# Kernel tuning notes

Measured on AMD Instinct MI355X. Metric: run time of the kernel, lower is better.

Reference implementation:

```python
import jax, jax.numpy as jnp
import numpy as np

RHO = 1.0
EPSILON = 0.1
N_ITERS = 5
EPS = 1e-08


def setup_inputs() -> dict:
    key = jax.random.key(0)
    k1, k2, k3 = jax.random.split(key, 3)
    B, H, M, N, D = 16, 16, 256, 576, 1024
    # student cross-attention weights: positive, rows roughly sum to 1 (post-softmax in the real model)
    sa = jax.random.uniform(k1, (B, H, M, N), dtype=jnp.float32) + 1e-3
    student_attn = sa / sa.sum(axis=-1, keepdims=True)
    visual_feats = jax.random.normal(k2, (B, N, D), dtype=jnp.float32)
    text_feats = jax.random.normal(k3, (B, M, D), dtype=jnp.float32)
    text_mask = jnp.ones((B, M), dtype=jnp.float32)
    return {"student_attn": student_attn, "visual_feats": visual_feats,
            "text_feats": text_feats, "text_mask": text_mask}


def _l2norm(x):
    return x / jnp.sqrt(jnp.sum(x * x, axis=-1, keepdims=True) + 1e-12)


def _teacher_plan(x, y, y_mask):
    # x: (B,N,D) visual, y: (B,M,D) text, y_mask: (B,M)
    B, N, D = x.shape
    M = y.shape[1]
    x_n = _l2norm(x)
    y_n = _l2norm(y)
    cost = 1.0 - jnp.einsum('bmd,bnd->bmn', y_n, x_n)          # (B,M,N)
    mu = jnp.full((B, N, 1), 1.0 / N, dtype=x.dtype)            # visual marginal (column vec)
    nu = (y_mask / (jnp.sum(y_mask, axis=1, keepdims=True) + EPS))[:, :, None]  # (B,M,1)
    K = jnp.exp(-cost / EPSILON)                                # (B,M,N)
    fi = RHO / (RHO + EPSILON)
    u = jnp.ones((B, M, 1), dtype=x.dtype)
    v = jnp.ones((B, N, 1), dtype=x.dtype)
    for _ in range(N_ITERS):
        Kv = jnp.einsum('bmn,bnk->bmk', K, v)                   # (B,M,1)
        u = (nu / (Kv + EPS)) ** fi
        Ktu = jnp.einsum('bmn,bmk->bnk', K, u)                  # (B,N,1)
        v = (mu / (Ktu + EPS)) ** fi
    P = u * K * jnp.swapaxes(v, 1, 2)                           # (B,M,N)
    return P / (jnp.sum(P, axis=-1, keepdims=True) + EPS)


def reference(student_attn, visual_feats, text_feats, text_mask):
    teacher = jax.lax.stop_gradient(_teacher_plan(visual_feats, text_feats, text_mask))
    teacher = teacher[:, None, :, :]                            # (B,1,M,N)
    loss = -jnp.sum(teacher * jnp.log(student_attn + EPS), axis=-1)  # (B,H,M)
    loss = loss * text_mask[:, None, :]
    return jnp.mean(loss)
```

## Files before the change

### kernel.cpp

```cpp
#include <hip/hip_runtime.h>
#include <math.h>

#define B_ 16
#define H_ 16
#define M_ 256
#define N_ 576
#define D_ 1024
#define BK 64
#define LDS_STRIDE (BK + 8)
#define NROWS (B_ * N_ + B_ * M_)

constexpr float EPS_ = 1e-8f;
constexpr float FI_ = 0.90909090909090906f;

typedef __bf16 bf16x8 __attribute__((ext_vector_type(8)));
typedef float f32x4 __attribute__((ext_vector_type(4)));

__device__ __forceinline__ float wave_reduce(float v) {
#pragma unroll
  for (int o = 32; o > 0; o >>= 1) v += __shfl_down(v, o, 64);
  return v;
}

__device__ __forceinline__ unsigned short f2bf(float f) {
  union { float f; unsigned u; } a; a.f = f;
  unsigned r = a.u + 0x7fff + ((a.u >> 16) & 1);
  return (unsigned short)(r >> 16);
}

__device__ __forceinline__ float bf2f(unsigned short u) {
  union { unsigned u; float f; } a; a.u = ((unsigned)u) << 16;
  return a.f;
}

__global__ __launch_bounds__(256) void sumlog_kernel(const float* __restrict__ student,
                                                     float* __restrict__ SL) {
  const int m = blockIdx.x;
  const int b = blockIdx.y;
  const int t = threadIdx.x;
  if (t >= N_ / 4) return;
  const float* st = student + ((size_t)b * H_ * M_ + m) * N_ + t * 4;
  float4 acc = {0.f, 0.f, 0.f, 0.f};
#pragma unroll
  for (int h = 0; h < H_; ++h) {
    float4 s4 = *(const float4*)&st[(size_t)h * M_ * N_];
    acc.x += __logf(s4.x + EPS_);
    acc.y += __logf(s4.y + EPS_);
    acc.z += __logf(s4.z + EPS_);
    acc.w += __logf(s4.w + EPS_);
  }
  *(float4*)&SL[((size_t)b * M_ + m) * N_ + t * 4] = acc;
}

__global__ __launch_bounds__(256) void prep_kernel(const float* __restrict__ vis,
                                                   const float* __restrict__ txt,
                                                   const float* __restrict__ mask,
                                                   unsigned short* __restrict__ xb,
                                                   unsigned short* __restrict__ yb,
                                                   float* __restrict__ masksum) {
  const int bid = blockIdx.x;
  const int lane = threadIdx.x & 63;
  if (bid < NROWS / 4) {
    int wave = bid * 4 + (threadIdx.x >> 6);
    const float* src;
    unsigned short* dst;
    if (wave < B_ * N_) {
      src = vis + (size_t)wave * D_;
      dst = xb + (size_t)wave * D_;
    } else {
      int r = wave - B_ * N_;
      src = txt + (size_t)r * D_;
      dst = yb + (size_t)r * D_;
    }
    float4 v[4];
    float s = 0.f;
#pragma unroll
    for (int it = 0; it < 4; ++it) {
      v[it] = *(const float4*)&src[it * 256 + lane * 4];
      s += v[it].x * v[it].x + v[it].y * v[it].y + v[it].z * v[it].z + v[it].w * v[it].w;
    }
    s = wave_reduce(s);
    s = __shfl(s, 0, 64);
    float inv = rsqrtf(s + 1e-12f);
#pragma unroll
    for (int it = 0; it < 4; ++it) {
      ushort4 pk;
      pk.x = f2bf(v[it].x * inv);
      pk.y = f2bf(v[it].y * inv);
      pk.z = f2bf(v[it].z * inv);
      pk.w = f2bf(v[it].w * inv);
      *(ushort4*)&dst[it * 256 + lane * 4] = pk;
    }
  } else {
    int b = (bid - NROWS / 4) * 4 + (threadIdx.x >> 6);
    float4 mv = *(const float4*)&mask[b * M_ + lane * 4];
    float s = wave_reduce(mv.x + mv.y + mv.z + mv.w);
    if (lane == 0) masksum[b] = s;
  }
}

__global__ __launch_bounds__(256) void gemm_k_mfma(const unsigned short* __restrict__ xb,
                                                   const unsigned short* __restrict__ yb,
                                                   unsigned short* __restrict__ Kw) {
  __shared__ unsigned short As[64][LDS_STRIDE];
  __shared__ unsigned short Bs[64][LDS_STRIDE];
  const int b = blockIdx.z;
  const int m0 = blockIdx.y * 64;
  const int n0 = blockIdx.x * 64;
  const unsigned short* Y = yb + (size_t)b * M_ * D_;
  const unsigned short* X = xb + (size_t)b * N_ * D_;
  const int t = threadIdx.x;
  const int lane = t & 63;
  const int w = t >> 6;
  const int wm = (w & 1) * 32;
  const int wn = (w >> 1) * 32;
  const int lr = t >> 3;
  const int lc = (t & 7) * 8;
  const int fr = lane & 15;
  const int fk = (lane >> 4) * 8;

  f32x4 acc[2][2] = {};
  for (int k0 = 0; k0 < D_; k0 += BK) {
#pragma unroll
    for (int p = 0; p < 2; ++p) {
      *(uint4*)&As[lr + 32 * p][lc] = *(const uint4*)&Y[(size_t)(m0 + lr + 32 * p) * D_ + k0 + lc];
      *(uint4*)&Bs[lr + 32 * p][lc] = *(const uint4*)&X[(size_t)(n0 + lr + 32 * p) * D_ + k0 + lc];
    }
    __syncthreads();
#pragma unroll
    for (int ks = 0; ks < BK; ks += 32) {
      bf16x8 a[2], bfr[2];
#pragma unroll
      for (int i = 0; i < 2; ++i) {
        a[i] = *(const bf16x8*)&As[wm + i * 16 + fr][ks + fk];
        bfr[i] = *(const bf16x8*)&Bs[wn + i * 16 + fr][ks + fk];
      }
#pragma unroll
      for (int i = 0; i < 2; ++i)
#pragma unroll
        for (int j = 0; j < 2; ++j)
          acc[i][j] = __builtin_amdgcn_mfma_f32_16x16x32_bf16(a[i], bfr[j], acc[i][j], 0, 0, 0);
    }
    __syncthreads();
  }

  const int cm = (lane >> 4) * 4;
  const int cn = lane & 15;
#pragma unroll
  for (int i = 0; i < 2; ++i)
#pragma unroll
    for (int j = 0; j < 2; ++j)
#pragma unroll
      for (int rg = 0; rg < 4; ++rg) {
        int m = m0 + wm + i * 16 + cm + rg;
        int n = n0 + wn + j * 16 + cn;
        Kw[((size_t)b * M_ + m) * N_ + n] = f2bf(expf(10.f * (acc[i][j][rg] - 1.f)));
      }
}


__global__ __launch_bounds__(256) void sink_u_first(const unsigned short* __restrict__ Kw,
                                                    const float* __restrict__ mask,
                                                    const float* __restrict__ masksum,
                                                    float* __restrict__ u) {
  const int b = blockIdx.y;
  const int row = blockIdx.x * 4 + (threadIdx.x >> 6);
  const int lane = threadIdx.x & 63;
  const unsigned short* rowp = Kw + ((size_t)b * M_ + row) * N_;
  float s = 0.f;
#pragma unroll
  for (int k = 0; k < 9; ++k) s += bf2f(rowp[lane + 64 * k]);
  s = wave_reduce(s);
  if (lane == 0) {
    int idx = b * M_ + row;
    float nu = mask[idx] / (masksum[b] + EPS_);
    u[idx] = powf(nu / (s + EPS_), FI_);
  }
}

__global__ __launch_bounds__(256) void sink_u(const unsigned short* __restrict__ Kw,
                                              const float* __restrict__ v,
                                              const float* __restrict__ mask,
                                              const float* __restrict__ masksum,
                                              float* __restrict__ u) {
  const int b = blockIdx.y;
  const int row = blockIdx.x * 4 + (threadIdx.x >> 6);
  const int lane = threadIdx.x & 63;
  const unsigned short* rowp = Kw + ((size_t)b * M_ + row) * N_;
  const float* vb = v + b * N_;
  float s = 0.f;
#pragma unroll
  for (int k = 0; k < 9; ++k) s += bf2f(rowp[lane + 64 * k]) * vb[lane + 64 * k];
  s = wave_reduce(s);
  if (lane == 0) {
    int idx = b * M_ + row;
    float nu = mask[idx] / (masksum[b] + EPS_);
    u[idx] = powf(nu / (s + EPS_), FI_);
  }
}

__global__ __launch_bounds__(256) void sink_v(const unsigned short* __restrict__ Kw,
                                              const float* __restrict__ u,
                                              float* __restrict__ v) {
  __shared__ float part[4][64];
  const int b = blockIdx.y;
  const int n0 = blockIdx.x * 64;
  const int col = n0 + (threadIdx.x & 63);
  const int g = threadIdx.x >> 6;
  const unsigned short* Kb = Kw + (size_t)b * M_ * N_;
  const float* ub = u + b * M_;
  float s = 0.f;
#pragma unroll 8
  for (int m = g * 64; m < (g + 1) * 64; ++m) s += bf2f(Kb[(size_t)m * N_ + col]) * ub[m];
  part[g][threadIdx.x & 63] = s;
  __syncthreads();
  if (threadIdx.x < 64) {
    float tot = part[0][threadIdx.x] + part[1][threadIdx.x] +
                part[2][threadIdx.x] + part[3][threadIdx.x];
    v[b * N_ + n0 + threadIdx.x] = powf((1.f / (float)N_) / (tot + EPS_), FI_);
  }
}

__global__ __launch_bounds__(256) void finloss_kernel(const unsigned short* __restrict__ Kw,
                                                      const float* __restrict__ SL,
                                                      const float* __restrict__ v,
                                                      const float* __restrict__ mask,
                                                      float* __restrict__ partial) {
  __shared__ float red[2][4];
  const int m = blockIdx.x;
  const int b = blockIdx.y;
  const int t = threadIdx.x;
  float s1 = 0.f, s2 = 0.f;
  if (t < N_ / 4) {
    const unsigned short* kp = Kw + ((size_t)b * M_ + m) * N_ + t * 4;
    ushort4 k4 = *(const ushort4*)kp;
    float4 v4 = *(const float4*)&v[b * N_ + t * 4];
    float4 sl4 = *(const float4*)&SL[((size_t)b * M_ + m) * N_ + t * 4];
    float kv0 = bf2f(k4.x) * v4.x, kv1 = bf2f(k4.y) * v4.y;
    float kv2 = bf2f(k4.z) * v4.z, kv3 = bf2f(k4.w) * v4.w;
    s1 = kv0 + kv1 + kv2 + kv3;
    s2 = kv0 * sl4.x + kv1 * sl4.y + kv2 * sl4.z + kv3 * sl4.w;
  }
  s1 = wave_reduce(s1);
  s2 = wave_reduce(s2);
  if ((t & 63) == 0) { red[0][t >> 6] = s1; red[1][t >> 6] = s2; }
  __syncthreads();
  if (t == 0) {
    float S1 = red[0][0] + red[0][1] + red[0][2] + red[0][3];
    float S2 = red[1][0] + red[1][1] + red[1][2] + red[1][3];
    int row = b * M_ + m;
    partial[row] = -mask[row] * S2 / ((S1 + EPS_) * (float)(B_ * H_ * M_));
  }
}

__global__ __launch_bounds__(256) void reduce_kernel(const float* __restrict__ partial,
                                                     float* __restrict__ out) {
  __shared__ float red[4];
  float s = 0.f;
  for (int i = threadIdx.x; i < B_ * M_; i += 256) s += partial[i];
  s = wave_reduce(s);
  if ((threadIdx.x & 63) == 0) red[threadIdx.x >> 6] = s;
  __syncthreads();
  if (threadIdx.x == 0) out[0] = red[0] + red[1] + red[2] + red[3];
}

extern "C" void kernel_launch(void* const* d_in, const int* in_sizes, int n_in,
                              void* d_out, int out_size, void* d_ws, size_t ws_size,
                              hipStream_t stream) {
  const float* student = (const float*)d_in[0];
  const float* vis = (const float*)d_in[1];
  const float* txt = (const float*)d_in[2];
  const float* mask = (const float*)d_in[3];
  float* out = (float*)d_out;

  char* p = (char*)d_ws;
  unsigned short* Kb = (unsigned short*)p; p += (size_t)B_ * M_ * N_ * 2;
  unsigned short* xb = (unsigned short*)p; p += (size_t)B_ * N_ * D_ * 2;
  unsigned short* yb = (unsigned short*)p; p += (size_t)B_ * M_ * D_ * 2;
  float* SL = (float*)p;      p += (size_t)B_ * M_ * N_ * 4;
  float* vv = (float*)p;      p += B_ * N_ * 4;
  float* uu = (float*)p;      p += B_ * M_ * 4;
  float* msum = (float*)p;    p += B_ * 4;
  float* partial = (float*)p; p += B_ * M_ * 4;

  sumlog_kernel<<<dim3(M_, B_), 256, 0, stream>>>(student, SL);

  prep_kernel<<<NROWS / 4 + 4, 256, 0, stream>>>(vis, txt, mask, xb, yb, msum);
  gemm_k_mfma<<<dim3(N_ / 64, M_ / 64, B_), 256, 0, stream>>>(xb, yb, Kb);

  sink_u_first<<<dim3(M_ / 4, B_), 256, 0, stream>>>(Kb, mask, msum, uu);
  sink_v<<<dim3(N_ / 64, B_), 256, 0, stream>>>(Kb, uu, vv);
  for (int it = 1; it < 5; ++it) {
    sink_u<<<dim3(M_ / 4, B_), 256, 0, stream>>>(Kb, vv, mask, msum, uu);
    sink_v<<<dim3(N_ / 64, B_), 256, 0, stream>>>(Kb, uu, vv);
  }

  finloss_kernel<<<dim3(M_, B_), 256, 0, stream>>>(Kb, SL, vv, mask, partial);
  reduce_kernel<<<1, 256, 0, stream>>>(partial, out);
}
```

Before: 335.7 us.

## Fuse Sinkhorn iterations into one per-batch kernel co-scheduled with sumlog

Replaces the ten separate Sinkhorn u/v kernel launches with a single kernel in which one 1024-thread block per batch runs all five iterations, keeping u and v in shared memory. The student log-sum work moves into extra blocks of the same launch, so it runs alongside the serial Sinkhorn blocks instead of as its own kernel. This removes launch overhead and global round-trips for u and v. In exchange only 16 blocks do the Sinkhorn work, which leaves little parallelism per batch, and the sumlog part now runs after the GEMM rather than before it.

```diff
diff --git a/kernel.cpp b/kernel.cpp
--- a/kernel.cpp
+++ b/kernel.cpp
@@ -10,6 +10,9 @@
 #define LDS_STRIDE (BK + 8)
 #define NROWS (B_ * N_ + B_ * M_)
 
+#define SINK_BLOCKS B_
+#define SUMLOG_BLOCKS ((B_ * M_ * N_ / 4) / 1024)
+
 constexpr float EPS_ = 1e-8f;
 constexpr float FI_ = 0.90909090909090906f;
 
@@ -31,25 +34,6 @@
 __device__ __forceinline__ float bf2f(unsigned short u) {
   union { unsigned u; float f; } a; a.u = ((unsigned)u) << 16;
   return a.f;
-}
-
-__global__ __launch_bounds__(256) void sumlog_kernel(const float* __restrict__ student,
-                                                     float* __restrict__ SL) {
-  const int m = blockIdx.x;
-  const int b = blockIdx.y;
-  const int t = threadIdx.x;
-  if (t >= N_ / 4) return;
-  const float* st = student + ((size_t)b * H_ * M_ + m) * N_ + t * 4;
-  float4 acc = {0.f, 0.f, 0.f, 0.f};
-#pragma unroll
-  for (int h = 0; h < H_; ++h) {
-    float4 s4 = *(const float4*)&st[(size_t)h * M_ * N_];
-    acc.x += __logf(s4.x + EPS_);
-    acc.y += __logf(s4.y + EPS_);
-    acc.z += __logf(s4.z + EPS_);
-    acc.w += __logf(s4.w + EPS_);
-  }
-  *(float4*)&SL[((size_t)b * M_ + m) * N_ + t * 4] = acc;
 }
 
 __global__ __launch_bounds__(256) void prep_kernel(const float* __restrict__ vis,
@@ -158,67 +142,83 @@
       }
 }
 
-
-__global__ __launch_bounds__(256) void sink_u_first(const unsigned short* __restrict__ Kw,
-                                                    const float* __restrict__ mask,
-                                                    const float* __restrict__ masksum,
-                                                    float* __restrict__ u) {
-  const int b = blockIdx.y;
-  const int row = blockIdx.x * 4 + (threadIdx.x >> 6);
-  const int lane = threadIdx.x & 63;
-  const unsigned short* rowp = Kw + ((size_t)b * M_ + row) * N_;
-  float s = 0.f;
-#pragma unroll
-  for (int k = 0; k < 9; ++k) s += bf2f(rowp[lane + 64 * k]);
-  s = wave_reduce(s);
-  if (lane == 0) {
-    int idx = b * M_ + row;
-    float nu = mask[idx] / (masksum[b] + EPS_);
-    u[idx] = powf(nu / (s + EPS_), FI_);
-  }
-}
-
-__global__ __launch_bounds__(256) void sink_u(const unsigned short* __restrict__ Kw,
-                                              const float* __restrict__ v,
-                                              const float* __restrict__ mask,
-                                              const float* __restrict__ masksum,
-                                              float* __restrict__ u) {
-  const int b = blockIdx.y;
-  const int row = blockIdx.x * 4 + (threadIdx.x >> 6);
-  const int lane = threadIdx.x & 63;
-  const unsigned short* rowp = Kw + ((size_t)b * M_ + row) * N_;
-  const float* vb = v + b * N_;
-  float s = 0.f;
-#pragma unroll
-  for (int k = 0; k < 9; ++k) s += bf2f(rowp[lane + 64 * k]) * vb[lane + 64 * k];
-  s = wave_reduce(s);
-  if (lane == 0) {
-    int idx = b * M_ + row;
-    float nu = mask[idx] / (masksum[b] + EPS_);
-    u[idx] = powf(nu / (s + EPS_), FI_);
-  }
-}
-
-__global__ __launch_bounds__(256) void sink_v(const unsigned short* __restrict__ Kw,
-                                              const float* __restrict__ u,
-                                              float* __restrict__ v) {
-  __shared__ float part[4][64];
-  const int b = blockIdx.y;
-  const int n0 = blockIdx.x * 64;
-  const int col = n0 + (threadIdx.x & 63);
-  const int g = threadIdx.x >> 6;
+__global__ __launch_bounds__(1024) void sink_sumlog_kernel(
+    const unsigned short* __restrict__ Kw,
+    const float* __restrict__ mask,
+    const float* __restrict__ masksum,
+    const float* __restrict__ student,
+    float* __restrict__ SL,
+    float* __restrict__ vv) {
+  if (blockIdx.x >= SINK_BLOCKS) {
+    const int t = threadIdx.x;
+    const int idx = (blockIdx.x - SINK_BLOCKS) * 1024 + t;
+    const int b = idx / (M_ * N_ / 4);
+    const int cb = idx - b * (M_ * N_ / 4);
+    const float* st = student + (size_t)b * H_ * M_ * N_ + (size_t)cb * 4;
+    float4 acc = {0.f, 0.f, 0.f, 0.f};
+#pragma unroll
+    for (int h = 0; h < H_; ++h) {
+      float4 s4 = *(const float4*)&st[(size_t)h * M_ * N_];
+      acc.x += __logf(s4.x + EPS_);
+      acc.y += __logf(s4.y + EPS_);
+      acc.z += __logf(s4.z + EPS_);
+      acc.w += __logf(s4.w + EPS_);
+    }
+    *(float4*)&SL[(size_t)b * M_ * N_ + (size_t)cb * 4] = acc;
+    return;
+  }
+
+  __shared__ float u_s[M_];
+  __shared__ float v_s[N_];
+  __shared__ float nu_s[M_];
+  __shared__ float vp[4][N_];
+  const int b = blockIdx.x;
+  const int t = threadIdx.x;
+  const int lane = t & 63;
+  const int w = t >> 6;
   const unsigned short* Kb = Kw + (size_t)b * M_ * N_;
-  const float* ub = u + b * M_;
-  float s = 0.f;
+
+  if (t < M_) nu_s[t] = mask[b * M_ + t] / (masksum[b] + EPS_);
+  if (t < N_) v_s[t] = 1.f;
+  __syncthreads();
+
+  for (int it = 0; it < 5; ++it) {
+#pragma unroll 2
+    for (int r = 0; r < 16; ++r) {
+      const int m = w * 16 + r;
+      const unsigned short* rp = Kb + (size_t)m * N_;
+      float s = 0.f;
+#pragma unroll
+      for (int k = 0; k < 9; ++k) s += bf2f(rp[lane + 64 * k]) * v_s[lane + 64 * k];
+      s = wave_reduce(s);
+      if (lane == 0) u_s[m] = powf(nu_s[m] / (s + EPS_), FI_);
+    }
+    __syncthreads();
+
+    if (t < 576) {
+      const int q = t / 144;
+      const int c4 = (t - q * 144) * 4;
+      float s0 = 0.f, s1 = 0.f, s2 = 0.f, s3 = 0.f;
 #pragma unroll 8
-  for (int m = g * 64; m < (g + 1) * 64; ++m) s += bf2f(Kb[(size_t)m * N_ + col]) * ub[m];
-  part[g][threadIdx.x & 63] = s;
-  __syncthreads();
-  if (threadIdx.x < 64) {
-    float tot = part[0][threadIdx.x] + part[1][threadIdx.x] +
-                part[2][threadIdx.x] + part[3][threadIdx.x];
-    v[b * N_ + n0 + threadIdx.x] = powf((1.f / (float)N_) / (tot + EPS_), FI_);
-  }
+      for (int m = q * 64; m < q * 64 + 64; ++m) {
+        ushort4 k4 = *(const ushort4*)&Kb[(size_t)m * N_ + c4];
+        const float um = u_s[m];
+        s0 += bf2f(k4.x) * um;
+        s1 += bf2f(k4.y) * um;
+        s2 += bf2f(k4.z) * um;
+        s3 += bf2f(k4.w) * um;
+      }
+      float4 r4 = {s0, s1, s2, s3};
+      *(float4*)&vp[q][c4] = r4;
+    }
+    __syncthreads();
+    if (t < N_) {
+      float tot = vp[0][t] + vp[1][t] + vp[2][t] + vp[3][t];
+      v_s[t] = powf((1.f / (float)N_) / (tot + EPS_), FI_);
+    }
+    __syncthreads();
+  }
+  if (t < N_) vv[b * N_ + t] = v_s[t];
 }
 
 __global__ __launch_bounds__(256) void finloss_kernel(const unsigned short* __restrict__ Kw,
@@ -279,21 +279,14 @@
   unsigned short* yb = (unsigned short*)p; p += (size_t)B_ * M_ * D_ * 2;
   float* SL = (float*)p;      p += (size_t)B_ * M_ * N_ * 4;
   float* vv = (float*)p;      p += B_ * N_ * 4;
-  float* uu = (float*)p;      p += B_ * M_ * 4;
   float* msum = (float*)p;    p += B_ * 4;
   float* partial = (float*)p; p += B_ * M_ * 4;
 
-  sumlog_kernel<<<dim3(M_, B_), 256, 0, stream>>>(student, SL);
-
   prep_kernel<<<NROWS / 4 + 4, 256, 0, stream>>>(vis, txt, mask, xb, yb, msum);
   gemm_k_mfma<<<dim3(N_ / 64, M_ / 64, B_), 256, 0, stream>>>(xb, yb, Kb);
 
-  sink_u_first<<<dim3(M_ / 4, B_), 256, 0, stream>>>(Kb, mask, msum, uu);
-  sink_v<<<dim3(N_ / 64, B_), 256, 0, stream>>>(Kb, uu, vv);
-  for (int it = 1; it < 5; ++it) {
-    sink_u<<<dim3(M_ / 4, B_), 256, 0, stream>>>(Kb, vv, mask, msum, uu);
-    sink_v<<<dim3(N_ / 64, B_), 256, 0, stream>>>(Kb, uu, vv);
-  }
+  sink_sumlog_kernel<<<SINK_BLOCKS + SUMLOG_BLOCKS, 1024, 0, stream>>>(
+      Kb, mask, msum, student, SL, vv);
 
   finloss_kernel<<<dim3(M_, B_), 256, 0, stream>>>(Kb, SL, vv, mask, partial);
   reduce_kernel<<<1, 256, 0, stream>>>(partial, out);
```

After: 399.0 us. +18.9%, slower.

## Fold student log-sum work into Sinkhorn iteration kernels as extra blocks

Applied to the files above, without the earlier changes.

Removes the standalone sumlog kernel and spreads its 4096 row units across the ten Sinkhorn kernels, each launched with extra blocks that each compute one sum-of-logs row. The goal is to fill the mostly idle GPU during the small, latency-bound Sinkhorn launches with the bandwidth-heavy student read. The risk is that the extra blocks lengthen each serial iteration kernel. The ten chunks of 410 units cover all 4096 rows before finloss reads SL.

```diff
diff --git a/kernel.cpp b/kernel.cpp
--- a/kernel.cpp
+++ b/kernel.cpp
@@ -10,6 +10,9 @@
 #define LDS_STRIDE (BK + 8)
 #define NROWS (B_ * N_ + B_ * M_)
 
+#define SL_TOTAL (B_ * M_)
+#define SL_CHUNK 410
+
 constexpr float EPS_ = 1e-8f;
 constexpr float FI_ = 0.90909090909090906f;
 
@@ -33,12 +36,12 @@
   return a.f;
 }
 
-__global__ __launch_bounds__(256) void sumlog_kernel(const float* __restrict__ student,
-                                                     float* __restrict__ SL) {
-  const int m = blockIdx.x;
-  const int b = blockIdx.y;
-  const int t = threadIdx.x;
+__device__ __forceinline__ void sumlog_unit(const float* __restrict__ student,
+                                            float* __restrict__ SL, int unit,
+                                            int t) {
   if (t >= N_ / 4) return;
+  const int b = unit >> 8;
+  const int m = unit & 255;
   const float* st = student + ((size_t)b * H_ * M_ + m) * N_ + t * 4;
   float4 acc = {0.f, 0.f, 0.f, 0.f};
 #pragma unroll
@@ -162,7 +165,16 @@
 __global__ __launch_bounds__(256) void sink_u_first(const unsigned short* __restrict__ Kw,
                                                     const float* __restrict__ mask,
                                                     const float* __restrict__ masksum,
-                                                    float* __restrict__ u) {
+                                                    float* __restrict__ u,
+                                                    const float* __restrict__ student,
+                                                    float* __restrict__ SL, int chunk) {
+  if (blockIdx.x >= M_ / 4) {
+    const int idx = (blockIdx.x - M_ / 4) * B_ + blockIdx.y;
+    const int unit = chunk * SL_CHUNK + idx;
+    if (idx < SL_CHUNK && unit < SL_TOTAL)
+      sumlog_unit(student, SL, unit, threadIdx.x);
+    return;
+  }
   const int b = blockIdx.y;
   const int row = blockIdx.x * 4 + (threadIdx.x >> 6);
   const int lane = threadIdx.x & 63;
@@ -182,7 +194,16 @@
                                               const float* __restrict__ v,
                                               const float* __restrict__ mask,
                                               const float* __restrict__ masksum,
-                                              float* __restrict__ u) {
+                                              float* __restrict__ u,
+                                              const float* __restrict__ student,
+                                              float* __restrict__ SL, int chunk) {
+  if (blockIdx.x >= M_ / 4) {
+    const int idx = (blockIdx.x - M_ / 4) * B_ + blockIdx.y;
+    const int unit = chunk * SL_CHUNK + idx;
+    if (idx < SL_CHUNK && unit < SL_TOTAL)
+      sumlog_unit(student, SL, unit, threadIdx.x);
+    return;
+  }
   const int b = blockIdx.y;
   const int row = blockIdx.x * 4 + (threadIdx.x >> 6);
   const int lane = threadIdx.x & 63;
@@ -201,7 +222,16 @@
 
 __global__ __launch_bounds__(256) void sink_v(const unsigned short* __restrict__ Kw,
                                               const float* __restrict__ u,
-                                              float* __restrict__ v) {
+                                              float* __restrict__ v,
+                                              const float* __restrict__ student,
+                                              float* __restrict__ SL, int chunk) {
+  if (blockIdx.x >= N_ / 64) {
+    const int idx = (blockIdx.x - N_ / 64) * B_ + blockIdx.y;
+    const int unit = chunk * SL_CHUNK + idx;
+    if (idx < SL_CHUNK && unit < SL_TOTAL)
+      sumlog_unit(student, SL, unit, threadIdx.x);
+    return;
+  }
   __shared__ float part[4][64];
   const int b = blockIdx.y;
   const int n0 = blockIdx.x * 64;
@@ -283,16 +313,19 @@
   float* msum = (float*)p;    p += B_ * 4;
   float* partial = (float*)p; p += B_ * M_ * 4;
 
-  sumlog_kernel<<<dim3(M_, B_), 256, 0, stream>>>(student, SL);
+  const int UXTRA = (SL_CHUNK + B_ - 1) / B_;
 
   prep_kernel<<<NROWS / 4 + 4, 256, 0, stream>>>(vis, txt, mask, xb, yb, msum);
   gemm_k_mfma<<<dim3(N_ / 64, M_ / 64, B_), 256, 0, stream>>>(xb, yb, Kb);
 
-  sink_u_first<<<dim3(M_ / 4, B_), 256, 0, stream>>>(Kb, mask, msum, uu);
-  sink_v<<<dim3(N_ / 64, B_), 256, 0, stream>>>(Kb, uu, vv);
+  sink_u_first<<<dim3(M_ / 4 + UXTRA, B_), 256, 0, stream>>>(Kb, mask, msum, uu,
+                                                             student, SL, 0);
+  sink_v<<<dim3(N_ / 64 + UXTRA, B_), 256, 0, stream>>>(Kb, uu, vv, student, SL, 1);
   for (int it = 1; it < 5; ++it) {
-    sink_u<<<dim3(M_ / 4, B_), 256, 0, stream>>>(Kb, vv, mask, msum, uu);
-    sink_v<<<dim3(N_ / 64, B_), 256, 0, stream>>>(Kb, uu, vv);
+    sink_u<<<dim3(M_ / 4 + UXTRA, B_), 256, 0, stream>>>(Kb, vv, mask, msum, uu,
+                                                         student, SL, 2 * it);
+    sink_v<<<dim3(N_ / 64 + UXTRA, B_), 256, 0, stream>>>(Kb, uu, vv, student, SL,
+                                                          2 * it + 1);
   }
 
   finloss_kernel<<<dim3(M_, B_), 256, 0, stream>>>(Kb, SL, vv, mask, partial);
```

New measurement: 337.6 us. No clear change (+0.6%).
